# Kernel tuning notes

Hardware: AMD Instinct MI355X
Metric: run time of the kernel (lower is better)

The kernel has to match this reference:

```python
import jax, jax.numpy as jnp
import numpy as np

B, N, T, CIN = 16, 400, 12, 2
HID, H, D = 256, 8, 32
P, EMB, TOPK, K = 3, 10, 16, 3


def _conv1d(x, w, b, dil):
    # x: (BN, C, T), w: (O, I, K); causal (left) padding like F.pad((pad,0))
    pad = (K - 1) * dil
    y = jax.lax.conv_general_dilated(x, w, (1,), [(pad, 0)], rhs_dilation=(dil,),
                                     dimension_numbers=('NCH', 'OIH', 'NCH'))
    return y + b[None, :, None]


def _ln(x, g, b):
    m = x.mean(-1, keepdims=True)
    v = x.var(-1, keepdims=True)
    return (x - m) / jnp.sqrt(v + 1e-5) * g + b


def setup_inputs() -> dict:
    key = jax.random.key(0)
    kit = iter(jax.random.split(key, 64))

    def g(shape, s=0.05):
        return jax.random.normal(next(kit), shape, jnp.float32) * s

    # fixed graph: ring with 8 neighbors + self loop -> L = 9*N edges
    idx = np.arange(N)
    offs = np.array([-4, -3, -2, -1, 0, 1, 2, 3, 4])
    recv = np.repeat(idx, offs.size)
    send = (recv + np.tile(offs, N)) % N
    L = recv.size

    inp = {
        'x': g((B, N, T, CIN), 1.0),
        'edge_feat': g((B, L, 2), 1.0),
        'fixed_edge_index': jnp.asarray(np.stack([recv, send]).astype(np.int32)),
        # GTCN layer 0 (dilation 1): gate/filter/skip convs + LayerNorm
        'wg0': g((HID, CIN, K)), 'bg0': jnp.zeros((HID,), jnp.float32),
        'wf0': g((HID, CIN, K)), 'bf0': jnp.zeros((HID,), jnp.float32),
        'ws0': g((HID, CIN, K)), 'bs0': jnp.zeros((HID,), jnp.float32),
        'ln0g': jnp.ones((HID,), jnp.float32), 'ln0b': jnp.zeros((HID,), jnp.float32),
        # GTCN layer 1 (dilation 2)
        'wg1': g((HID, HID, K)), 'bg1': jnp.zeros((HID,), jnp.float32),
        'wf1': g((HID, HID, K)), 'bf1': jnp.zeros((HID,), jnp.float32),
        'ws1': g((HID, HID, K)), 'bs1': jnp.zeros((HID,), jnp.float32),
        'ln1g': jnp.ones((HID,), jnp.float32), 'ln1b': jnp.zeros((HID,), jnp.float32),
        'wsk': g((CIN, HID)), 'bsk': jnp.zeros((HID,), jnp.float32),
        # sparse GAT on fixed physical graph (with 2-dim edge features)
        'sWq': g((HID, HID)), 'sWk': g((HID, HID)), 'sWv': g((HID, HID)),
        'sWe': g((2, HID)),
        'saq': g((H, D)), 'sak': g((H, D)), 'sae': g((H, D)),
        # dense GAT on adaptive adjacency
        'dWq': g((HID, HID)), 'dWk': g((HID, HID)), 'dWv': g((HID, HID)),
        'daq': g((H, D)), 'dak': g((H, D)),
        'E1': g((N, EMB), 0.5), 'E2': g((N, EMB), 0.5),
        # gated fusion
        'fW1': g((HID, HID)), 'fb1': jnp.zeros((HID,), jnp.float32),
        'fW2': g((HID, HID)), 'fb2': jnp.zeros((HID,), jnp.float32),
        'fW3': g((HID, HID)), 'fb3': jnp.zeros((HID,), jnp.float32),
        # prediction head
        'Wo': g((HID, P)), 'bo': jnp.zeros((P,), jnp.float32),
    }
    return inp


def reference(x, edge_feat,
              wg0, bg0, wf0, bf0, ws0, bs0, ln0g, ln0b,
              wg1, bg1, wf1, bf1, ws1, bs1, ln1g, ln1b, wsk, bsk,
              sWq, sWk, sWv, sWe, saq, sak, sae,
              dWq, dWk, dWv, daq, dak, E1, E2,
              fW1, fb1, fW2, fb2, fW3, fb3, Wo, bo,
              fixed_edge_index):
    Bb, Nn, Tt, _ = x.shape
    # ---- GTCN (gated temporal conv stack with residual skip) ----
    res = x @ wsk + bsk                                   # (B,N,T,HID)
    xc = x.reshape(Bb * Nn, Tt, -1).transpose(0, 2, 1)    # (BN,C,T)
    for (wg, bg, wf, bf, ws, bs, lg, lb), dil in (
            ((wg0, bg0, wf0, bf0, ws0, bs0, ln0g, ln0b), 1),
            ((wg1, bg1, wf1, bf1, ws1, bs1, ln1g, ln1b), 2)):
        gate = jax.nn.sigmoid(_conv1d(xc, wg, bg, dil))
        y = gate * _conv1d(xc, wf, bf, dil) + (1 - gate) * _conv1d(xc, ws, bs, dil)
        y = jax.nn.relu(_ln(y.transpose(0, 2, 1), lg, lb))  # (BN,T,HID)
        xc = y.transpose(0, 2, 1)
    h = xc.transpose(0, 2, 1).reshape(Bb, Nn, Tt, HID) + res
    hl = h[:, :, -1, :]                                   # (B,N,HID) last step

    # ---- sparse GAT on fixed physical graph (edge features) ----
    recv, send = fixed_edge_index[0], fixed_edge_index[1]
    q = (hl @ sWq).reshape(Bb, Nn, H, D)
    k = (hl @ sWk).reshape(Bb, Nn, H, D)
    v = (hl @ sWv).reshape(Bb, Nn, H, D)
    e = (edge_feat @ sWe).reshape(Bb, -1, H, D)
    s = (q[:, recv] * saq).sum(-1) + (k[:, send] * sak).sum(-1) + (e * sae).sum(-1)
    s = jax.nn.leaky_relu(s, 0.2)                         # (B,L,H)
    mx = jnp.full((Bb, Nn, H), -jnp.inf, s.dtype).at[:, recv].max(s)
    ex = jnp.exp(s - mx[:, recv])
    den = jnp.zeros((Bb, Nn, H), s.dtype).at[:, recv].add(ex)
    alpha = ex / jnp.clip(den[:, recv], 1e-12, None)
    agg = jnp.zeros((Bb, Nn, H, D), v.dtype).at[:, recv].add(alpha[..., None] * v[:, send])
    h_fixed = jax.nn.elu(agg.reshape(Bb, Nn, HID))

    # ---- dense GAT on adaptive (learned, top-k sparsified) adjacency ----
    A = jax.nn.softmax(jax.nn.relu(E1 @ E2.T), axis=-1)   # (N,N)
    kth = jax.lax.top_k(A, TOPK)[0][:, -1:]
    adj_adp = jnp.where(A >= kth, A, 0.0)
    q = (hl @ dWq).reshape(Bb, Nn, H, D)
    k = (hl @ dWk).reshape(Bb, Nn, H, D)
    v = (hl @ dWv).reshape(Bb, Nn, H, D)
    sc = (q * daq).sum(-1)[:, :, None, :] + (k * dak).sum(-1)[:, None, :, :]  # (B,N,N,H)
    sc = jax.nn.leaky_relu(sc, 0.2)
    sc = sc + jnp.log(jnp.clip(adj_adp, 1e-12, None))[None, :, :, None]      # log-adj trick
    sc = jnp.where((adj_adp > 0)[None, :, :, None], sc, -1e9)
    al = jax.nn.softmax(sc, axis=2)
    h_adp = jax.nn.elu(jnp.einsum('bnjh,bjhd->bnhd', al, v).reshape(Bb, Nn, HID))

    # ---- gated fusion + prediction head ----
    gate = jax.nn.sigmoid((h_fixed + h_adp) @ fW1 + fb1)
    fused = jnp.tanh(gate * (h_fixed @ fW2 + fb2) + (1 - gate) * (h_adp @ fW3 + fb3))
    return fused @ Wo + bo                                # (B,N,P)
```

## Files before the change

kernel.cpp:

```cpp
#include <hip/hip_runtime.h>
#include <math.h>

#define LL 3600
#define NODES 6400

typedef __attribute__((ext_vector_type(8))) _Float16 half8;
typedef __attribute__((ext_vector_type(4))) float f32x4;

__device__ __forceinline__ unsigned short f2h(float f) {
    union { _Float16 h; unsigned short u; } cv;
    cv.h = (_Float16)f;
    return cv.u;
}
__device__ __forceinline__ float h2f(unsigned short u) {
    union { unsigned short u; _Float16 h; } cv;
    cv.u = u;
    return (float)cv.h;
}

#define GLOAD16(gp, lp) __builtin_amdgcn_global_load_lds( \
    (const __attribute__((address_space(1))) unsigned int*)(const void*)(gp), \
    (__attribute__((address_space(3))) unsigned int*)(void*)(lp), 16, 0, 0)

__global__ __launch_bounds__(256) void prep_kernel(
    const float* __restrict__ wg1, const float* __restrict__ wf1, const float* __restrict__ ws1,
    const float* __restrict__ sWv, const float* __restrict__ dWv,
    const float* __restrict__ sWq, const float* __restrict__ saq,
    const float* __restrict__ sWk, const float* __restrict__ sak,
    const float* __restrict__ dWq, const float* __restrict__ daq,
    const float* __restrict__ dWk, const float* __restrict__ dak,
    const float* __restrict__ fW1, const float* __restrict__ fW2, const float* __restrict__ fW3,
    const float* __restrict__ sWe, const float* __restrict__ sae,
    const float* __restrict__ E1, const float* __restrict__ E2,
    const float* __restrict__ x,
    const float* __restrict__ wg0, const float* __restrict__ bg0,
    const float* __restrict__ wf0, const float* __restrict__ bf0,
    const float* __restrict__ ws0, const float* __restrict__ bs0,
    const float* __restrict__ lg0, const float* __restrict__ lb0,
    unsigned short* __restrict__ W1h,
    unsigned short* __restrict__ W2h,
    unsigned short* __restrict__ W3h,
    float* __restrict__ AeS,
    int* __restrict__ cnt, int* __restrict__ idxs, float* __restrict__ logv,
    unsigned short* __restrict__ Xh) {
    int bid = blockIdx.x;
    int tid = threadIdx.x;

    if (bid < 2304) {
        int idx = bid * 256 + tid;
        int n = idx / 768, k = idx % 768;
        int which = n >> 8, o = n & 255;
        int tt = k >> 8, i = k & 255;
        const float* w = which == 0 ? wg1 : (which == 1 ? wf1 : ws1);
        W1h[idx] = f2h(w[(o * 256 + i) * 3 + tt]);
    } else if (bid < 2944) {
        int idx = (bid - 2304) * 256 + tid;
        int n = idx / 256, k = idx % 256;
        float v = 0.f;
        if (n < 256) v = sWv[k * 256 + n];
        else if (n < 512) v = dWv[k * 256 + (n - 256)];
        else if (n < 544) {
            int j = n - 512, g = j >> 3, h = j & 7;
            const float* Wm = g == 0 ? sWq : (g == 1 ? sWk : (g == 2 ? dWq : dWk));
            const float* am = g == 0 ? saq : (g == 1 ? sak : (g == 2 ? daq : dak));
            float s = 0.f;
            for (int d = 0; d < 32; d++) s += Wm[k * 256 + h * 32 + d] * am[h * 32 + d];
            v = s;
        }
        W2h[idx] = f2h(v);
    } else if (bid < 4480) {
        int idx = (bid - 2944) * 256 + tid;
        int n = idx / 512, k = idx % 512;
        float v = 0.f;
        if (k < 256) {
            if (n < 256) v = fW1[k * 256 + n];
            else if (n < 512) v = fW2[k * 256 + (n - 256)];
        } else {
            int c = k - 256;
            if (n < 256) v = fW1[c * 256 + n];
            else if (n >= 512) v = fW3[c * 256 + (n - 512)];
        }
        W3h[idx] = f2h(v);
    } else if (bid == 4480) {
        if (tid < 16) {
            int cc = tid / 8, h = tid % 8;
            float s = 0.f;
            for (int d = 0; d < 32; d++) s += sWe[cc * 256 + h * 32 + d] * sae[h * 32 + d];
            AeS[tid] = s;
        }
    } else if (bid < 4581) {
        int n = ((bid - 4481) * 256 + tid) >> 6;
        int lane = tid & 63;
        if (n >= 400) return;
        float e1[10];
        #pragma unroll
        for (int k = 0; k < 10; k++) e1[k] = E1[n * 10 + k];
        float p[7];
        #pragma unroll
        for (int i = 0; i < 7; i++) {
            int j = i * 64 + lane;
            if (j < 400) {
                float s = 0.f;
                #pragma unroll
                for (int k = 0; k < 10; k++) s += e1[k] * E2[j * 10 + k];
                p[i] = fmaxf(s, 0.f);
            } else p[i] = -1e30f;
        }
        float mx = -1e30f;
        #pragma unroll
        for (int i = 0; i < 7; i++) mx = fmaxf(mx, p[i]);
        #pragma unroll
        for (int o = 32; o > 0; o >>= 1) mx = fmaxf(mx, __shfl_xor(mx, o, 64));
        float sum = 0.f;
        #pragma unroll
        for (int i = 0; i < 7; i++) {
            int j = i * 64 + lane;
            if (j < 400) { p[i] = expf(p[i] - mx); sum += p[i]; }
        }
        #pragma unroll
        for (int o = 32; o > 0; o >>= 1) sum += __shfl_xor(sum, o, 64);
        float inv = 1.f / sum;
        float m[7];
        #pragma unroll
        for (int i = 0; i < 7; i++) {
            int j = i * 64 + lane;
            if (j < 400) { p[i] *= inv; m[i] = p[i]; }
            else m[i] = -1e30f;
        }
        for (int it = 0; it < 15; ++it) {
            float lm = m[0];
            #pragma unroll
            for (int i = 1; i < 7; i++) lm = fmaxf(lm, m[i]);
            float gm = lm;
            #pragma unroll
            for (int o = 32; o > 0; o >>= 1) gm = fmaxf(gm, __shfl_xor(gm, o, 64));
            unsigned long long msk = __ballot(lm == gm);
            int first = (int)(__ffsll((long long)msk)) - 1;
            if (lane == first) {
                #pragma unroll
                for (int i = 0; i < 7; i++) {
                    if (m[i] == gm) { m[i] = -1e30f; break; }
                }
            }
        }
        float kth = m[0];
        #pragma unroll
        for (int i = 1; i < 7; i++) kth = fmaxf(kth, m[i]);
        #pragma unroll
        for (int o = 32; o > 0; o >>= 1) kth = fmaxf(kth, __shfl_xor(kth, o, 64));
        int base = 0;
        #pragma unroll
        for (int i = 0; i < 7; i++) {
            int j = i * 64 + lane;
            bool pred = (j < 400) && (p[i] >= kth);
            unsigned long long msk = __ballot(pred);
            int pre = __popcll(msk & ((lane == 63) ? 0x7fffffffffffffffull : ((1ull << lane) - 1)));
            if (pred) {
                int pos = base + pre;
                if (pos < 64) {
                    idxs[n * 64 + pos] = j;
                    logv[n * 64 + pos] = logf(fmaxf(p[i], 1e-12f));
                }
            }
            base += __popcll(msk);
        }
        if (lane == 0) cnt[n] = base < 64 ? base : 64;
    } else {
        int lane = tid & 63;
        int node = (bid - 4581) * 4 + (tid >> 6);
        float xs[14];
        #pragma unroll
        for (int t = 0; t < 7; t++) {
            xs[t * 2]     = x[(size_t)(node * 12 + 5 + t) * 2];
            xs[t * 2 + 1] = x[(size_t)(node * 12 + 5 + t) * 2 + 1];
        }
        float wg[4][6], wf[4][6], wsv[4][6], bgv[4], bfv[4], bsv[4], gln[4], bln[4];
        #pragma unroll
        for (int cc = 0; cc < 4; cc++) {
            int o = lane * 4 + cc;
            #pragma unroll
            for (int i = 0; i < 6; i++) {
                wg[cc][i] = wg0[o * 6 + i];
                wf[cc][i] = wf0[o * 6 + i];
                wsv[cc][i] = ws0[o * 6 + i];
            }
            bgv[cc] = bg0[o]; bfv[cc] = bf0[o]; bsv[cc] = bs0[o];
            gln[cc] = lg0[o]; bln[cc] = lb0[o];
        }
        #pragma unroll
        for (int tt = 0; tt < 3; tt++) {
            int tb = 2 * tt;
            float y[4];
            float s1 = 0.f, s2 = 0.f;
            #pragma unroll
            for (int cc = 0; cc < 4; cc++) {
                float g = bgv[cc], f = bfv[cc], s = bsv[cc];
                #pragma unroll
                for (int k = 0; k < 3; k++) {
                    #pragma unroll
                    for (int c = 0; c < 2; c++) {
                        float xv = xs[(tb + k) * 2 + c];
                        g += wg[cc][c * 3 + k] * xv;
                        f += wf[cc][c * 3 + k] * xv;
                        s += wsv[cc][c * 3 + k] * xv;
                    }
                }
                float gate = 1.f / (1.f + expf(-g));
                y[cc] = gate * f + (1.f - gate) * s;
                s1 += y[cc];
                s2 += y[cc] * y[cc];
            }
            #pragma unroll
            for (int o = 32; o > 0; o >>= 1) {
                s1 += __shfl_xor(s1, o, 64);
                s2 += __shfl_xor(s2, o, 64);
            }
            float mean = s1 * (1.f / 256.f);
            float var = s2 * (1.f / 256.f) - mean * mean;
            float rstd = rsqrtf(var + 1e-5f);
            unsigned short h4[4];
            #pragma unroll
            for (int cc = 0; cc < 4; cc++) {
                float v = (y[cc] - mean) * rstd * gln[cc] + bln[cc];
                h4[cc] = f2h(fmaxf(v, 0.f));
            }
            unsigned long long pack = (unsigned long long)h4[0] | ((unsigned long long)h4[1] << 16)
                                    | ((unsigned long long)h4[2] << 32) | ((unsigned long long)h4[3] << 48);
            *(unsigned long long*)&Xh[(size_t)node * 768 + tt * 256 + lane * 4] = pack;
        }
    }
}

template<int K, int LDC, int GX>
__global__ __launch_bounds__(256, 6) void gemm_f16(
    const unsigned short* __restrict__ A,
    const unsigned short* __restrict__ BT,
    unsigned short* __restrict__ C) {
    __shared__ __align__(16) unsigned short lA[3][64 * 32];
    __shared__ __align__(16) unsigned short lB[3][64 * 32];
    int tid = threadIdx.x;
    int lane = tid & 63;
    int w = tid >> 6;
    int wm = w >> 1, wn = w & 1;
    int r = lane & 15, g4 = lane >> 4;

    constexpr int NWG = GX * 100;
    constexpr int Q = NWG / 8, R = NWG % 8;
    int flat = blockIdx.y * GX + blockIdx.x;
    int xcd = flat & 7, idx = flat >> 3;
    int nf = (xcd < R ? xcd * (Q + 1) : R * (Q + 1) + (xcd - R) * Q) + idx;
    int col0 = (nf % GX) * 64;
    int row0 = (nf / GX) * 64;

    f32x4 acc[2][2] = {};

    int rS = tid >> 2;
    int slot = tid & 3;
    int tk = (slot ^ (rS & 3)) * 8;

#define STAGE(sel, kk) do { \
    GLOAD16(A + (size_t)(row0 + rS) * K + (kk) + tk, &lA[sel][tid * 8]); \
    GLOAD16(BT + (size_t)(col0 + rS) * K + (kk) + tk, &lB[sel][tid * 8]); \
} while (0)

    int sw = (g4 ^ (r & 3)) << 3;

#define COMPUTE(cur) do { \
    half8 a_[2], b_[2]; \
    _Pragma("unroll") \
    for (int mi = 0; mi < 2; ++mi) \
        a_[mi] = *(const half8*)&lA[cur][(wm * 32 + mi * 16 + r) * 32 + sw]; \
    _Pragma("unroll") \
    for (int ni = 0; ni < 2; ++ni) \
        b_[ni] = *(const half8*)&lB[cur][(wn * 32 + ni * 16 + r) * 32 + sw]; \
    _Pragma("unroll") \
    for (int mi = 0; mi < 2; ++mi) \
        _Pragma("unroll") \
        for (int ni = 0; ni < 2; ++ni) \
            acc[mi][ni] = __builtin_amdgcn_mfma_f32_16x16x32_f16(a_[mi], b_[ni], acc[mi][ni], 0, 0, 0); \
} while (0)

    constexpr int NT = K >> 5;
    STAGE(0, 0);
    STAGE(1, 32);
    for (int t = 0; t < NT - 1; ++t) {
        asm volatile("s_waitcnt vmcnt(2)" ::: "memory");
        __builtin_amdgcn_s_barrier();
        if (t + 2 < NT) STAGE((t + 2) % 3, (t + 2) * 32);
        COMPUTE(t % 3);
    }
    asm volatile("s_waitcnt vmcnt(0)" ::: "memory");
    __builtin_amdgcn_s_barrier();
    COMPUTE((NT - 1) % 3);
#undef STAGE
#undef COMPUTE

    #pragma unroll
    for (int mi = 0; mi < 2; ++mi) {
        #pragma unroll
        for (int ni = 0; ni < 2; ++ni) {
            int rowb = row0 + wm * 32 + mi * 16 + g4 * 4;
            int colb = col0 + wn * 32 + ni * 16 + r;
            #pragma unroll
            for (int j = 0; j < 4; ++j)
                C[(size_t)(rowb + j) * LDC + colb] = f2h(acc[mi][ni][j]);
        }
    }
}

__global__ __launch_bounds__(256) void epi1_kernel(
    const unsigned short* __restrict__ Y1, const float* __restrict__ x,
    const float* __restrict__ bg1, const float* __restrict__ bf1, const float* __restrict__ bs1,
    const float* __restrict__ lg, const float* __restrict__ lb,
    const float* __restrict__ wsk, const float* __restrict__ bsk,
    unsigned short* __restrict__ HLh) {
    int node = blockIdx.x, o = threadIdx.x;
    __shared__ float red[8];
    size_t base = (size_t)node * 768;
    float g = h2f(Y1[base + o]) + bg1[o];
    float f = h2f(Y1[base + 256 + o]) + bf1[o];
    float s = h2f(Y1[base + 512 + o]) + bs1[o];
    float gate = 1.f / (1.f + expf(-g));
    float y = gate * f + (1.f - gate) * s;
    float a = y, bb = y * y;
    #pragma unroll
    for (int off = 32; off > 0; off >>= 1) { a += __shfl_xor(a, off, 64); bb += __shfl_xor(bb, off, 64); }
    int w = o >> 6, l = o & 63;
    if (l == 0) { red[w] = a; red[4 + w] = bb; }
    __syncthreads();
    float sum = red[0] + red[1] + red[2] + red[3];
    float sq = red[4] + red[5] + red[6] + red[7];
    float mean = sum * (1.f / 256.f);
    float var = sq * (1.f / 256.f) - mean * mean;
    float v = (y - mean) * rsqrtf(var + 1e-5f) * lg[o] + lb[o];
    v = fmaxf(v, 0.f);
    float x0 = x[(size_t)(node * 12 + 11) * 2];
    float x1 = x[(size_t)(node * 12 + 11) * 2 + 1];
    float res = x0 * wsk[o] + x1 * wsk[256 + o] + bsk[o];
    HLh[(size_t)node * 256 + o] = f2h(v + res);
}

__global__ __launch_bounds__(256) void gat_kernel(
    const unsigned short* __restrict__ Y2, const float* __restrict__ ef,
    const int* __restrict__ fei, const float* __restrict__ AeS,
    const int* __restrict__ cnt, const int* __restrict__ idxs, const float* __restrict__ logv,
    unsigned short* __restrict__ Uh) {
    int node = blockIdx.x;
    int b = node / 400, n = node % 400;
    int tid = threadIdx.x;
    __shared__ int snd[9];
    __shared__ float alf[9][8];
    __shared__ float invdf[8];
    __shared__ int jidx[64];
    __shared__ float sca[64][8];
    __shared__ float alb[64][8];
    __shared__ float invda[8];
    __shared__ float svf[9][8];
    int c = cnt[n];

    if (tid < 64) {
        int lane = tid;
        if (lane < 9) snd[lane] = fei[LL + n * 9 + lane];
        for (int e = lane; e < 72; e += 64) {
            int j = e >> 3, h = e & 7;
            int l = n * 9 + j;
            float e0 = ef[((size_t)b * LL + l) * 2];
            float e1 = ef[((size_t)b * LL + l) * 2 + 1];
            float ae = e0 * AeS[h] + e1 * AeS[8 + h];
            float aq = h2f(Y2[(size_t)node * 640 + 512 + h]);
            float ak = h2f(Y2[((size_t)(b * 400 + snd[j])) * 640 + 520 + h]);
            float s = aq + ak + ae;
            svf[j][h] = s > 0.f ? s : 0.2f * s;
        }
        if (lane < 8) {
            int h = lane;
            float mx = -1e30f;
            #pragma unroll
            for (int j = 0; j < 9; j++) mx = fmaxf(mx, svf[j][h]);
            float den = 0.f;
            #pragma unroll
            for (int j = 0; j < 9; j++) { float e = expf(svf[j][h] - mx); alf[j][h] = e; den += e; }
            invdf[h] = 1.f / fmaxf(den, 1e-12f);
        }
    } else if (tid < 128) {
        int lane = tid - 64;
        if (lane < c) jidx[lane] = idxs[n * 64 + lane];
        float jl = (lane < c) ? logv[n * 64 + lane] : 0.f;
        for (int e = lane; e < c * 8; e += 64) {
            int j = e >> 3, h = e & 7;
            float aq = h2f(Y2[(size_t)node * 640 + 528 + h]);
            float ak = h2f(Y2[((size_t)(b * 400 + jidx[j])) * 640 + 536 + h]);
            float s = aq + ak;
            s = s > 0.f ? s : 0.2f * s;
            sca[j][h] = s + __shfl(jl, j, 64);
        }
        int h = lane >> 3, grp = lane & 7;
        float mx = -1e30f;
        for (int j = grp; j < c; j += 8) mx = fmaxf(mx, sca[j][h]);
        #pragma unroll
        for (int o = 1; o < 8; o <<= 1) mx = fmaxf(mx, __shfl_xor(mx, o, 64));
        float s = 0.f;
        for (int j = grp; j < c; j += 8) { float e = expf(sca[j][h] - mx); alb[j][h] = e; s += e; }
        #pragma unroll
        for (int o = 1; o < 8; o <<= 1) s += __shfl_xor(s, o, 64);
        if (grp == 0) invda[h] = 1.f / s;
    }
    __syncthreads();

    if (tid < 128) {
        int ch = tid * 2;
        int h = ch >> 5;
        float a0 = 0.f, a1 = 0.f;
        #pragma unroll
        for (int j = 0; j < 9; j++) {
            unsigned v = *(const unsigned*)&Y2[((size_t)(b * 400 + snd[j])) * 640 + ch];
            float al = alf[j][h];
            a0 += al * h2f((unsigned short)(v & 0xffff));
            a1 += al * h2f((unsigned short)(v >> 16));
        }
        float iv = invdf[h];
        a0 *= iv; a1 *= iv;
        a0 = a0 > 0.f ? a0 : (expf(a0) - 1.f);
        a1 = a1 > 0.f ? a1 : (expf(a1) - 1.f);
        unsigned o = (unsigned)f2h(a0) | ((unsigned)f2h(a1) << 16);
        *(unsigned*)&Uh[(size_t)node * 512 + ch] = o;
    } else {
        int ch = (tid - 128) * 2;
        int h = ch >> 5;
        float a0 = 0.f, a1 = 0.f;
        for (int j = 0; j < c; j++) {
            unsigned v = *(const unsigned*)&Y2[((size_t)(b * 400 + jidx[j])) * 640 + 256 + ch];
            float al = alb[j][h];
            a0 += al * h2f((unsigned short)(v & 0xffff));
            a1 += al * h2f((unsigned short)(v >> 16));
        }
        float iv = invda[h];
        a0 *= iv; a1 *= iv;
        a0 = a0 > 0.f ? a0 : (expf(a0) - 1.f);
        a1 = a1 > 0.f ? a1 : (expf(a1) - 1.f);
        unsigned o = (unsigned)f2h(a0) | ((unsigned)f2h(a1) << 16);
        *(unsigned*)&Uh[(size_t)node * 512 + 256 + ch] = o;
    }
}

__global__ __launch_bounds__(256) void final_kernel(
    const unsigned short* __restrict__ Y3,
    const float* __restrict__ fb1, const float* __restrict__ fb2, const float* __restrict__ fb3,
    const float* __restrict__ Wo, const float* __restrict__ bo,
    float* __restrict__ out) {
    int node = blockIdx.x, o = threadIdx.x;
    __shared__ float red[12];
    size_t base = (size_t)node * 768;
    float g = 1.f / (1.f + expf(-(h2f(Y3[base + o]) + fb1[o])));
    float a2 = h2f(Y3[base + 256 + o]) + fb2[o];
    float a3 = h2f(Y3[base + 512 + o]) + fb3[o];
    float fused = tanhf(g * a2 + (1.f - g) * a3);
    float v0 = fused * Wo[o * 3 + 0];
    float v1 = fused * Wo[o * 3 + 1];
    float v2 = fused * Wo[o * 3 + 2];
    #pragma unroll
    for (int off = 32; off > 0; off >>= 1) {
        v0 += __shfl_xor(v0, off, 64);
        v1 += __shfl_xor(v1, off, 64);
        v2 += __shfl_xor(v2, off, 64);
    }
    int w = o >> 6, l = o & 63;
    if (l == 0) { red[w] = v0; red[4 + w] = v1; red[8 + w] = v2; }
    __syncthreads();
    if (o < 3) {
        float s = red[o * 4] + red[o * 4 + 1] + red[o * 4 + 2] + red[o * 4 + 3];
        out[(size_t)node * 3 + o] = s + bo[o];
    }
}

extern "C" void kernel_launch(void* const* d_in, const int* in_sizes, int n_in,
                              void* d_out, int out_size, void* d_ws, size_t ws_size,
                              hipStream_t stream) {
    const float* x   = (const float*)d_in[0];
    const float* ef  = (const float*)d_in[1];
    const int*   fei = (const int*)d_in[2];
    const float* wg0 = (const float*)d_in[3];
    const float* bg0 = (const float*)d_in[4];
    const float* wf0 = (const float*)d_in[5];
    const float* bf0 = (const float*)d_in[6];
    const float* ws0 = (const float*)d_in[7];
    const float* bs0 = (const float*)d_in[8];
    const float* ln0g = (const float*)d_in[9];
    const float* ln0b = (const float*)d_in[10];
    const float* wg1 = (const float*)d_in[11];
    const float* bg1 = (const float*)d_in[12];
    const float* wf1 = (const float*)d_in[13];
    const float* bf1 = (const float*)d_in[14];
    const float* ws1 = (const float*)d_in[15];
    const float* bs1 = (const float*)d_in[16];
    const float* ln1g = (const float*)d_in[17];
    const float* ln1b = (const float*)d_in[18];
    const float* wsk = (const float*)d_in[19];
    const float* bsk = (const float*)d_in[20];
    const float* sWq = (const float*)d_in[21];
    const float* sWk = (const float*)d_in[22];
    const float* sWv = (const float*)d_in[23];
    const float* sWe = (const float*)d_in[24];
    const float* saq = (const float*)d_in[25];
    const float* sak = (const float*)d_in[26];
    const float* sae = (const float*)d_in[27];
    const float* dWq = (const float*)d_in[28];
    const float* dWk = (const float*)d_in[29];
    const float* dWv = (const float*)d_in[30];
    const float* daq = (const float*)d_in[31];
    const float* dak = (const float*)d_in[32];
    const float* E1  = (const float*)d_in[33];
    const float* E2  = (const float*)d_in[34];
    const float* fW1 = (const float*)d_in[35];
    const float* fb1 = (const float*)d_in[36];
    const float* fW2 = (const float*)d_in[37];
    const float* fb2 = (const float*)d_in[38];
    const float* fW3 = (const float*)d_in[39];
    const float* fb3 = (const float*)d_in[40];
    const float* Wo  = (const float*)d_in[41];
    const float* bo  = (const float*)d_in[42];
    float* out = (float*)d_out;

    char* b = (char*)d_ws;
    unsigned short* Xh  = (unsigned short*)(b + 0);
    unsigned short* Yh  = (unsigned short*)(b + 9830400);
    unsigned short* HLh = (unsigned short*)(b + 19660800);
    unsigned short* Uh  = (unsigned short*)(b + 22937600);
    unsigned short* W1h = (unsigned short*)(b + 29491200);
    unsigned short* W2h = (unsigned short*)(b + 30670848);
    unsigned short* W3h = (unsigned short*)(b + 30998528);
    float*          AES = (float*)(b + 31784960);
    float*          LOGV= (float*)(b + 31785216);
    int*            CNT = (int*)(b + 31887616);
    int*            IDX = (int*)(b + 31889216);

    prep_kernel<<<6181, 256, 0, stream>>>(
        wg1, wf1, ws1,
        sWv, dWv, sWq, saq, sWk, sak, dWq, daq, dWk, dak,
        fW1, fW2, fW3, sWe, sae, E1, E2,
        x, wg0, bg0, wf0, bf0, ws0, bs0, ln0g, ln0b,
        W1h, W2h, W3h, AES,
        CNT, IDX, LOGV, Xh);

    gemm_f16<768, 768, 12><<<dim3(12, 100), 256, 0, stream>>>(Xh, W1h, Yh);

    epi1_kernel<<<NODES, 256, 0, stream>>>(Yh, x, bg1, bf1, bs1, ln1g, ln1b, wsk, bsk, HLh);

    gemm_f16<256, 640, 10><<<dim3(10, 100), 256, 0, stream>>>(HLh, W2h, Yh);

    gat_kernel<<<NODES, 256, 0, stream>>>(Yh, ef, fei, AES, CNT, IDX, LOGV, Uh);

    gemm_f16<512, 768, 12><<<dim3(12, 100), 256, 0, stream>>>(Uh, W3h, Yh);

    final_kernel<<<NODES, 256, 0, stream>>>(Yh, fb1, fb2, fb3, Wo, bo, out);
}
```

Before: 100.1 us.

## Fuse final gated-fusion head into third GEMM epilogue with atomic output reduction

Replaces the third GEMM and the separate final kernel with one kernel. Each block computes the matching gate, W2 and W3 column tiles together, then applies sigmoid/tanh fusion and the Wo projection in registers, reducing across lanes and adding partial sums to the output with atomics. The output is pre-filled with the bias in the prep kernel. This removes the fp16 round trip of the intermediate through global memory and one launch, at the cost of more LDS per block, lower occupancy and nondeterministic float summation order. Separately, the second GEMM now launches only 9 column tiles, skipping the last, apparently unused padding tile.

```diff
diff --git a/kernel.cpp b/kernel.cpp
--- a/kernel.cpp
+++ b/kernel.cpp
@@ -37,12 +37,14 @@
     const float* __restrict__ wf0, const float* __restrict__ bf0,
     const float* __restrict__ ws0, const float* __restrict__ bs0,
     const float* __restrict__ lg0, const float* __restrict__ lb0,
+    const float* __restrict__ bo,
     unsigned short* __restrict__ W1h,
     unsigned short* __restrict__ W2h,
     unsigned short* __restrict__ W3h,
     float* __restrict__ AeS,
     int* __restrict__ cnt, int* __restrict__ idxs, float* __restrict__ logv,
-    unsigned short* __restrict__ Xh) {
+    unsigned short* __restrict__ Xh,
+    float* __restrict__ out) {
     int bid = blockIdx.x;
     int tid = threadIdx.x;
 
@@ -165,7 +167,7 @@
             base += __popcll(msk);
         }
         if (lane == 0) cnt[n] = base < 64 ? base : 64;
-    } else {
+    } else if (bid < 6181) {
         int lane = tid & 63;
         int node = (bid - 4581) * 4 + (tid >> 6);
         float xs[14];
@@ -228,6 +230,9 @@
                                     | ((unsigned long long)h4[2] << 32) | ((unsigned long long)h4[3] << 48);
             *(unsigned long long*)&Xh[(size_t)node * 768 + tt * 256 + lane * 4] = pack;
         }
+    } else {
+        int idx = (bid - 6181) * 256 + tid;
+        if (idx < NODES * 3) out[idx] = bo[idx % 3];
     }
 }
 
@@ -304,6 +309,117 @@
             #pragma unroll
             for (int j = 0; j < 4; ++j)
                 C[(size_t)(rowb + j) * LDC + colb] = f2h(acc[mi][ni][j]);
+        }
+    }
+}
+
+__global__ __launch_bounds__(256, 3) void gemm3_fused(
+    const unsigned short* __restrict__ A,
+    const unsigned short* __restrict__ BT,
+    const float* __restrict__ fb1, const float* __restrict__ fb2, const float* __restrict__ fb3,
+    const float* __restrict__ Wo,
+    float* __restrict__ out) {
+    __shared__ __align__(16) unsigned short lA[3][64 * 32];
+    __shared__ __align__(16) unsigned short lB[3][3][64 * 32];
+    int tid = threadIdx.x;
+    int lane = tid & 63;
+    int w = tid >> 6;
+    int wm = w >> 1, wn = w & 1;
+    int r = lane & 15, g4 = lane >> 4;
+
+    constexpr int NWG = 400;
+    constexpr int Q = NWG / 8;
+    int flat = blockIdx.y * 4 + blockIdx.x;
+    int xcd = flat & 7, idx = flat >> 3;
+    int nf = xcd * Q + idx;
+    int c0 = (nf % 4) * 64;
+    int row0 = (nf / 4) * 64;
+
+    f32x4 acc[3][2][2] = {};
+
+    int rS = tid >> 2;
+    int slot = tid & 3;
+    int tk = (slot ^ (rS & 3)) * 8;
+
+#define STAGE3(sel, kk) do { \
+    GLOAD16(A + (size_t)(row0 + rS) * 512 + (kk) + tk, &lA[sel][tid * 8]); \
+    GLOAD16(BT + (size_t)(c0 + rS) * 512 + (kk) + tk, &lB[sel][0][tid * 8]); \
+    GLOAD16(BT + (size_t)(c0 + 256 + rS) * 512 + (kk) + tk, &lB[sel][1][tid * 8]); \
+    GLOAD16(BT + (size_t)(c0 + 512 + rS) * 512 + (kk) + tk, &lB[sel][2][tid * 8]); \
+} while (0)
+
+    int sw = (g4 ^ (r & 3)) << 3;
+
+#define COMPUTE3(cur) do { \
+    half8 a_[2], b_[3][2]; \
+    _Pragma("unroll") \
+    for (int mi = 0; mi < 2; ++mi) \
+        a_[mi] = *(const half8*)&lA[cur][(wm * 32 + mi * 16 + r) * 32 + sw]; \
+    _Pragma("unroll") \
+    for (int q = 0; q < 3; ++q) \
+        _Pragma("unroll") \
+        for (int ni = 0; ni < 2; ++ni) \
+            b_[q][ni] = *(const half8*)&lB[cur][q][(wn * 32 + ni * 16 + r) * 32 + sw]; \
+    _Pragma("unroll") \
+    for (int q = 0; q < 3; ++q) \
+        _Pragma("unroll") \
+        for (int mi = 0; mi < 2; ++mi) \
+            _Pragma("unroll") \
+            for (int ni = 0; ni < 2; ++ni) \
+                acc[q][mi][ni] = __builtin_amdgcn_mfma_f32_16x16x32_f16(a_[mi], b_[q][ni], acc[q][mi][ni], 0, 0, 0); \
+} while (0)
+
+    constexpr int NT = 16;
+    STAGE3(0, 0);
+    STAGE3(1, 32);
+    for (int t = 0; t < NT - 1; ++t) {
+        asm volatile("s_waitcnt vmcnt(4)" ::: "memory");
+        __builtin_amdgcn_s_barrier();
+        if (t + 2 < NT) STAGE3((t + 2) % 3, (t + 2) * 32);
+        COMPUTE3(t % 3);
+    }
+    asm volatile("s_waitcnt vmcnt(0)" ::: "memory");
+    __builtin_amdgcn_s_barrier();
+    COMPUTE3((NT - 1) % 3);
+#undef STAGE3
+#undef COMPUTE3
+
+    #pragma unroll
+    for (int mi = 0; mi < 2; ++mi) {
+        float v0[4] = {}, v1[4] = {}, v2[4] = {};
+        #pragma unroll
+        for (int ni = 0; ni < 2; ++ni) {
+            int ch = c0 + wn * 32 + ni * 16 + r;
+            float b1 = fb1[ch], b2 = fb2[ch], b3 = fb3[ch];
+            float w0 = Wo[ch * 3 + 0], w1 = Wo[ch * 3 + 1], w2 = Wo[ch * 3 + 2];
+            #pragma unroll
+            for (int j = 0; j < 4; ++j) {
+                float g = 1.f / (1.f + expf(-(acc[0][mi][ni][j] + b1)));
+                float a2 = acc[1][mi][ni][j] + b2;
+                float a3 = acc[2][mi][ni][j] + b3;
+                float fused = tanhf(g * a2 + (1.f - g) * a3);
+                v0[j] += fused * w0;
+                v1[j] += fused * w1;
+                v2[j] += fused * w2;
+            }
+        }
+        #pragma unroll
+        for (int off = 1; off < 16; off <<= 1) {
+            #pragma unroll
+            for (int j = 0; j < 4; ++j) {
+                v0[j] += __shfl_xor(v0[j], off, 64);
+                v1[j] += __shfl_xor(v1[j], off, 64);
+                v2[j] += __shfl_xor(v2[j], off, 64);
+            }
+        }
+        if (r == 0) {
+            int rowb = row0 + wm * 32 + mi * 16 + g4 * 4;
+            #pragma unroll
+            for (int j = 0; j < 4; ++j) {
+                atomicAdd(&out[(size_t)(rowb + j) * 3 + 0], v0[j]);
+                atomicAdd(&out[(size_t)(rowb + j) * 3 + 1], v1[j]);
+                atomicAdd(&out[(size_t)(rowb + j) * 3 + 2], v2[j]);
+            }
         }
     }
 }
@@ -440,36 +556,6 @@
         a1 = a1 > 0.f ? a1 : (expf(a1) - 1.f);
         unsigned o = (unsigned)f2h(a0) | ((unsigned)f2h(a1) << 16);
         *(unsigned*)&Uh[(size_t)node * 512 + 256 + ch] = o;
-    }
-}
-
-__global__ __launch_bounds__(256) void final_kernel(
-    const unsigned short* __restrict__ Y3,
-    const float* __restrict__ fb1, const float* __restrict__ fb2, const float* __restrict__ fb3,
-    const float* __restrict__ Wo, const float* __restrict__ bo,
-    float* __restrict__ out) {
-    int node = blockIdx.x, o = threadIdx.x;
-    __shared__ float red[12];
-    size_t base = (size_t)node * 768;
-    float g = 1.f / (1.f + expf(-(h2f(Y3[base + o]) + fb1[o])));
-    float a2 = h2f(Y3[base + 256 + o]) + fb2[o];
-    float a3 = h2f(Y3[base + 512 + o]) + fb3[o];
-    float fused = tanhf(g * a2 + (1.f - g) * a3);
-    float v0 = fused * Wo[o * 3 + 0];
-    float v1 = fused * Wo[o * 3 + 1];
-    float v2 = fused * Wo[o * 3 + 2];
-    #pragma unroll
-    for (int off = 32; off > 0; off >>= 1) {
-        v0 += __shfl_xor(v0, off, 64);
-        v1 += __shfl_xor(v1, off, 64);
-        v2 += __shfl_xor(v2, off, 64);
-    }
-    int w = o >> 6, l = o & 63;
-    if (l == 0) { red[w] = v0; red[4 + w] = v1; red[8 + w] = v2; }
-    __syncthreads();
-    if (o < 3) {
-        float s = red[o * 4] + red[o * 4 + 1] + red[o * 4 + 2] + red[o * 4 + 3];
-        out[(size_t)node * 3 + o] = s + bo[o];
     }
 }
 
@@ -534,23 +620,21 @@
     int*            CNT = (int*)(b + 31887616);
     int*            IDX = (int*)(b + 31889216);
 
-    prep_kernel<<<6181, 256, 0, stream>>>(
+    prep_kernel<<<6256, 256, 0, stream>>>(
         wg1, wf1, ws1,
         sWv, dWv, sWq, saq, sWk, sak, dWq, daq, dWk, dak,
         fW1, fW2, fW3, sWe, sae, E1, E2,
-        x, wg0, bg0, wf0, bf0, ws0, bs0, ln0g, ln0b,
+        x, wg0, bg0, wf0, bf0, ws0, bs0, ln0g, ln0b, bo,
         W1h, W2h, W3h, AES,
-        CNT, IDX, LOGV, Xh);
+        CNT, IDX, LOGV, Xh, out);
 
     gemm_f16<768, 768, 12><<<dim3(12, 100), 256, 0, stream>>>(Xh, W1h, Yh);
 
     epi1_kernel<<<NODES, 256, 0, stream>>>(Yh, x, bg1, bf1, bs1, ln1g, ln1b, wsk, bsk, HLh);
 
-    gemm_f16<256, 640, 10><<<dim3(10, 100), 256, 0, stream>>>(HLh, W2h, Yh);
+    gemm_f16<256, 640, 9><<<dim3(9, 100), 256, 0, stream>>>(HLh, W2h, Yh);
 
     gat_kernel<<<NODES, 256, 0, stream>>>(Yh, ef, fei, AES, CNT, IDX, LOGV, Uh);
 
-    gemm_f16<512, 768, 12><<<dim3(12, 100), 256, 0, stream>>>(Uh, W3h, Yh);
-
-    final_kernel<<<NODES, 256, 0, stream>>>(Yh, fb1, fb2, fb3, Wo, bo, out);
-}
+    gemm3_fused<<<dim3(4, 100), 256, 0, stream>>>(Uh, W3h, fb1, fb2, fb3, Wo, out);
+}
```

Result: no change. 99.09 us (-1.0%).
